# Kernel optimization log

Measured on AMD Instinct MI355X. Metric: run time of the kernel, lower is better.

## Reference

```python
import jax, jax.numpy as jnp
import numpy as np

B, M, N = 4, 1024, 32768

def setup_inputs() -> dict:
    key = jax.random.key(0)
    k1, k2 = jax.random.split(key)
    keypoints = jax.random.normal(k1, (B, 3, M), dtype=jnp.float32)
    pc = jax.random.normal(k2, (B, 3, N), dtype=jnp.float32)
    return {"keypoints": keypoints, "pc": pc}

def reference(keypoints, pc):
    # Pairwise Euclidean distances via the expanded quadratic form:
    # ||k - p||^2 = ||k||^2 + ||p||^2 - 2 k.p  -> avoids the [B,3,M,N] tensor.
    k2 = jnp.sum(keypoints * keypoints, axis=1)            # [B, M]
    p2 = jnp.sum(pc * pc, axis=1)                          # [B, N]
    cross = jnp.einsum("bdm,bdn->bmn", keypoints, pc)     # [B, M, N]
    d2 = k2[:, :, None] + p2[:, None, :] - 2.0 * cross     # [B, M, N]
    dist = jnp.sqrt(jnp.maximum(d2, 0.0))
    min_dist = jnp.min(dist, axis=2)                       # [B, M]
    return jnp.mean(min_dist)
```

## Files before the change

### kernel.cpp

```cpp
#include <hip/hip_runtime.h>
#include <math.h>

#define BATCH 4
#define M 1024
#define N 32768
#define MG 16
#define NMG (M / MG)
#define CSPLIT 8
#define NPC (N / CSPLIT)
#define TPB 256
#define ROWS (BATCH * M)


__global__ __launch_bounds__(TPB) void p2p_main(
        const float* __restrict__ kp, const float* __restrict__ pc,
        float* __restrict__ pmin) {
    const int c  = blockIdx.x & (CSPLIT - 1);
    const int mg = (blockIdx.x >> 3) & (NMG - 1);
    const int b  = blockIdx.x >> 9;
    const int t  = threadIdx.x;

    const float* kpb = kp + (size_t)b * 3 * M + mg * MG;
    float skx[MG], sky[MG], skz[MG];
#pragma unroll
    for (int k = 0; k < MG; ++k) {
        skx[k] = kpb[k];
        sky[k] = kpb[M + k];
        skz[k] = kpb[2 * M + k];
    }

    float mq[MG];
#pragma unroll
    for (int k = 0; k < MG; ++k) mq[k] = -INFINITY;

    const float* pcb = pc + (size_t)b * 3 * N + c * NPC;
#pragma unroll 2
    for (int g = 0; g < NPC / (TPB * 4); ++g) {
        const int n = g * (TPB * 4) + t * 4;
        float4 X4 = *(const float4*)&pcb[n];
        float4 Y4 = *(const float4*)&pcb[N + n];
        float4 Z4 = *(const float4*)&pcb[2 * N + n];
        float xs[4] = {X4.x, X4.y, X4.z, X4.w};
        float ys[4] = {Y4.x, Y4.y, Y4.z, Y4.w};
        float zs[4] = {Z4.x, Z4.y, Z4.z, Z4.w};
        float w[4];
#pragma unroll
        for (int p = 0; p < 4; ++p)
            w[p] = -0.5f * fmaf(xs[p], xs[p],
                                fmaf(ys[p], ys[p], zs[p] * zs[p]));
#pragma unroll
        for (int k = 0; k < MG; ++k) {
            float q0 = fmaf(skz[k], zs[0], fmaf(sky[k], ys[0],
                        fmaf(skx[k], xs[0], w[0])));
            float q1 = fmaf(skz[k], zs[1], fmaf(sky[k], ys[1],
                        fmaf(skx[k], xs[1], w[1])));
            float q2 = fmaf(skz[k], zs[2], fmaf(sky[k], ys[2],
                        fmaf(skx[k], xs[2], w[2])));
            float q3 = fmaf(skz[k], zs[3], fmaf(sky[k], ys[3],
                        fmaf(skx[k], xs[3], w[3])));
            mq[k] = fmaxf(fmaxf(mq[k], q0), q1);
            mq[k] = fmaxf(fmaxf(mq[k], q2), q3);
        }
    }

    __shared__ float smax[MG][TPB + 1];
    __shared__ float s2[MG][17];
#pragma unroll
    for (int k = 0; k < MG; ++k) smax[k][t] = mq[k];
    __syncthreads();
    {
        const int r = t >> 4, s = t & 15;
        float m = smax[r][s * 16];
#pragma unroll
        for (int j = 1; j < 16; ++j) m = fmaxf(m, smax[r][s * 16 + j]);
        s2[r][s] = m;
    }
    __syncthreads();
    if (t < MG) {
        float m = s2[t][0];
#pragma unroll
        for (int j = 1; j < 16; ++j) m = fmaxf(m, s2[t][j]);
        float kx = kpb[t], ky = kpb[M + t], kz = kpb[2 * M + t];
        float k2 = fmaf(kx, kx, fmaf(ky, ky, kz * kz));
        float d2 = fmaxf(fmaf(-2.0f, m, k2), 0.0f);
        pmin[(size_t)(b * M + mg * MG + t) * CSPLIT + c] = d2;
    }
}

__global__ __launch_bounds__(1024) void p2p_tail(
        const float* __restrict__ pmin, float* __restrict__ out) {
    __shared__ float sbuf[16];
    const int t = threadIdx.x;
    float s = 0.f;
#pragma unroll
    for (int i = 0; i < ROWS / 1024; ++i) {
        int r = i * 1024 + t;
        float4 a = *(const float4*)&pmin[(size_t)r * CSPLIT];
        float4 bq = *(const float4*)&pmin[(size_t)r * CSPLIT + 4];
        float v = fminf(fminf(fminf(a.x, a.y), fminf(a.z, a.w)),
                        fminf(fminf(bq.x, bq.y), fminf(bq.z, bq.w)));
        s += sqrtf(v);
    }
#pragma unroll
    for (int off = 32; off > 0; off >>= 1) s += __shfl_down(s, off, 64);
    if ((t & 63) == 0) sbuf[t >> 6] = s;
    __syncthreads();
    if (t == 0) {
        float tot = 0.f;
#pragma unroll
        for (int w = 0; w < 16; ++w) tot += sbuf[w];
        out[0] = tot / (float)ROWS;
    }
}

extern "C" void kernel_launch(void* const* d_in, const int* in_sizes, int n_in,
                              void* d_out, int out_size, void* d_ws, size_t ws_size,
                              hipStream_t stream) {
    const float* kp = (const float*)d_in[0];
    const float* pc = (const float*)d_in[1];
    float* out = (float*)d_out;
    float* pmin = (float*)d_ws;

    p2p_main<<<BATCH * NMG * CSPLIT, TPB, 0, stream>>>(kp, pc, pmin);
    p2p_tail<<<1, 1024, 0, stream>>>(pmin, out);
}
```

Before: 72.09 us.

## Fuse main and tail kernels via cooperative launch with grid sync

Merges the distance kernel and the final mean-reduction kernel into one cooperative kernel: each block writes its partial minima, then a grid-wide sync runs, and block 0 reduces everything. Block size drops from 256 to 128, so each thread processes twice as many point chunks and the intra-block reductions are resized to match. The goal is to remove the second kernel launch and its gap, at the cost of a grid barrier and a slower tail done by only 128 threads using scalar atomic loads.

New measurement: 257.7 us. 257% more time.

```diff
diff --git a/kernel.cpp b/kernel.cpp
--- a/kernel.cpp
+++ b/kernel.cpp
@@ -1,5 +1,8 @@
 #include <hip/hip_runtime.h>
+#include <hip/hip_cooperative_groups.h>
 #include <math.h>
+
+namespace cg = cooperative_groups;
 
 #define BATCH 4
 #define M 1024
@@ -8,13 +11,13 @@
 #define NMG (M / MG)
 #define CSPLIT 8
 #define NPC (N / CSPLIT)
-#define TPB 256
+#define TPB 128
 #define ROWS (BATCH * M)
+#define GRID (BATCH * NMG * CSPLIT)
 
-
-__global__ __launch_bounds__(TPB) void p2p_main(
+__global__ __launch_bounds__(TPB) void p2p_fused(
         const float* __restrict__ kp, const float* __restrict__ pc,
-        float* __restrict__ pmin) {
+        float* __restrict__ pmin, float* __restrict__ out) {
     const int c  = blockIdx.x & (CSPLIT - 1);
     const int mg = (blockIdx.x >> 3) & (NMG - 1);
     const int b  = blockIdx.x >> 9;
@@ -64,12 +67,12 @@
     }
 
     __shared__ float smax[MG][TPB + 1];
-    __shared__ float s2[MG][17];
+    __shared__ float s2[MG][9];
 #pragma unroll
     for (int k = 0; k < MG; ++k) smax[k][t] = mq[k];
     __syncthreads();
     {
-        const int r = t >> 4, s = t & 15;
+        const int r = t >> 3, s = t & 7;
         float m = smax[r][s * 16];
 #pragma unroll
         for (int j = 1; j < 16; ++j) m = fmaxf(m, smax[r][s * 16 + j]);
@@ -79,37 +82,36 @@
     if (t < MG) {
         float m = s2[t][0];
 #pragma unroll
-        for (int j = 1; j < 16; ++j) m = fmaxf(m, s2[t][j]);
+        for (int j = 1; j < 8; ++j) m = fmaxf(m, s2[t][j]);
         float kx = kpb[t], ky = kpb[M + t], kz = kpb[2 * M + t];
         float k2 = fmaf(kx, kx, fmaf(ky, ky, kz * kz));
         float d2 = fmaxf(fmaf(-2.0f, m, k2), 0.0f);
         pmin[(size_t)(b * M + mg * MG + t) * CSPLIT + c] = d2;
     }
-}
 
-__global__ __launch_bounds__(1024) void p2p_tail(
-        const float* __restrict__ pmin, float* __restrict__ out) {
-    __shared__ float sbuf[16];
-    const int t = threadIdx.x;
-    float s = 0.f;
+    cg::this_grid().sync();
+
+    if (blockIdx.x == 0) {
+        __shared__ float sb[2];
+        float s = 0.f;
+#pragma unroll 4
+        for (int i = 0; i < ROWS / TPB; ++i) {
+            int r = i * TPB + t;
+            const float* prow = pmin + (size_t)r * CSPLIT;
+            float v = INFINITY;
 #pragma unroll
-    for (int i = 0; i < ROWS / 1024; ++i) {
-        int r = i * 1024 + t;
-        float4 a = *(const float4*)&pmin[(size_t)r * CSPLIT];
-        float4 bq = *(const float4*)&pmin[(size_t)r * CSPLIT + 4];
-        float v = fminf(fminf(fminf(a.x, a.y), fminf(a.z, a.w)),
-                        fminf(fminf(bq.x, bq.y), fminf(bq.z, bq.w)));
-        s += sqrtf(v);
-    }
+            for (int j = 0; j < CSPLIT; ++j) {
+                float u = __hip_atomic_load(&prow[j], __ATOMIC_RELAXED,
+                                            __HIP_MEMORY_SCOPE_AGENT);
+                v = fminf(v, u);
+            }
+            s += sqrtf(v);
+        }
 #pragma unroll
-    for (int off = 32; off > 0; off >>= 1) s += __shfl_down(s, off, 64);
-    if ((t & 63) == 0) sbuf[t >> 6] = s;
-    __syncthreads();
-    if (t == 0) {
-        float tot = 0.f;
-#pragma unroll
-        for (int w = 0; w < 16; ++w) tot += sbuf[w];
-        out[0] = tot / (float)ROWS;
+        for (int off = 32; off > 0; off >>= 1) s += __shfl_down(s, off, 64);
+        if ((t & 63) == 0) sb[t >> 6] = s;
+        __syncthreads();
+        if (t == 0) out[0] = (sb[0] + sb[1]) / (float)ROWS;
     }
 }
 
@@ -121,6 +123,7 @@
     float* out = (float*)d_out;
     float* pmin = (float*)d_ws;
 
-    p2p_main<<<BATCH * NMG * CSPLIT, TPB, 0, stream>>>(kp, pc, pmin);
-    p2p_tail<<<1, 1024, 0, stream>>>(pmin, out);
+    void* args[] = {(void*)&kp, (void*)&pc, (void*)&pmin, (void*)&out};
+    hipLaunchCooperativeKernel((const void*)p2p_fused, dim3(GRID), dim3(TPB),
+                               args, 0, stream);
 }
```
